# Optimization experiments

Hardware: AMD Instinct MI355X
Metric: run time of the kernel (lower is better)

## Reference

```python
import jax, jax.numpy as jnp
import numpy as np

HIDDEN = 1024
N_HEADS = 16
HEAD_DIM = HIDDEN // N_HEADS


def setup_inputs() -> dict:
    key = jax.random.key(0)
    ks = jax.random.split(key, 9)
    s = 1.0 / np.sqrt(HIDDEN)
    d = {"hidden_states": jax.random.normal(ks[0], (2, 2048, HIDDEN), dtype=jnp.float32)}
    for i, name in enumerate(["q", "k", "v", "o"]):
        d[f"W{name}"] = jax.random.uniform(ks[1 + 2 * i], (HIDDEN, HIDDEN), minval=-s, maxval=s, dtype=jnp.float32)
        d[f"b{name}"] = jax.random.uniform(ks[2 + 2 * i], (HIDDEN,), minval=-s, maxval=s, dtype=jnp.float32)
    return d


def reference(hidden_states, Wq, bq, Wk, bk, Wv, bv, Wo, bo):
    B, L, _ = hidden_states.shape

    def shape(x):  # (B, L, H*D) -> (B, H, L, D)
        return x.reshape(B, L, N_HEADS, HEAD_DIM).transpose(0, 2, 1, 3)

    q = shape(hidden_states @ Wq.T + bq)
    k = shape(hidden_states @ Wk.T + bk)
    v = shape(hidden_states @ Wv.T + bv)
    scores = jnp.einsum("bhqd,bhkd->bhqk", q, k) / jnp.sqrt(jnp.float32(HEAD_DIM))
    attn = jax.nn.softmax(scores, axis=-1)
    ctx = jnp.einsum("bhqk,bhkd->bhqd", attn, v)
    ctx = ctx.transpose(0, 2, 1, 3).reshape(B, L, HIDDEN)
    return ctx @ Wo.T + bo
```

## Files before the change

kernel.cpp:

```cpp
#include <hip/hip_runtime.h>
#include <hip/hip_bf16.h>
#include <stdint.h>

typedef __bf16 bf16_t;
typedef __bf16 bf16x8 __attribute__((ext_vector_type(8)));
typedef __bf16 bf16x4 __attribute__((ext_vector_type(4)));
typedef float  f32x4  __attribute__((ext_vector_type(4)));
typedef float  f32x16 __attribute__((ext_vector_type(16)));

__device__ __forceinline__ f32x4 mfma16(bf16x8 a, bf16x8 b, f32x4 c) {
    return __builtin_amdgcn_mfma_f32_16x16x32_bf16(a, b, c, 0, 0, 0);
}
__device__ __forceinline__ f32x16 mfma32(bf16x8 a, bf16x8 b, f32x16 c) {
    return __builtin_amdgcn_mfma_f32_32x32x16_bf16(a, b, c, 0, 0, 0);
}
__device__ __forceinline__ void gload16(const void* g, void* l) {
    __builtin_amdgcn_global_load_lds(
        (const __attribute__((address_space(1))) unsigned int*)g,
        (__attribute__((address_space(3))) unsigned int*)l, 16, 0, 0);
}
__device__ __forceinline__ unsigned cvtpk(float lo, float hi_) {
    unsigned r;
    asm("v_cvt_pk_bf16_f32 %0, %1, %2" : "=v"(r) : "v"(lo), "v"(hi_));
    return r;
}
__device__ __forceinline__ float fexp2(float x) {
    return __builtin_amdgcn_exp2f(x);
}

__global__ __launch_bounds__(256) void split_x(const float* __restrict__ in,
                                               bf16_t* __restrict__ hi, int n8) {
    int i = blockIdx.x * 256 + threadIdx.x;
    if (i >= n8) return;
    int row = i >> 7;
    int di = (i & ~3) | ((i & 3) ^ ((row >> 1) & 3));
    const float4* in4 = reinterpret_cast<const float4*>(in);
    float4 v0 = in4[2 * i], v1 = in4[2 * i + 1];
    float vv[8] = {v0.x, v0.y, v0.z, v0.w, v1.x, v1.y, v1.z, v1.w};
    bf16x8 h;
#pragma unroll
    for (int j = 0; j < 8; ++j) h[j] = (bf16_t)vv[j];
    reinterpret_cast<bf16x8*>(hi)[di] = h;
}

__global__ __launch_bounds__(256) void split_w(const float* __restrict__ w0, const float* __restrict__ w1,
                                               const float* __restrict__ w2, const float* __restrict__ w3,
                                               bf16_t* __restrict__ h0, bf16_t* __restrict__ h1,
                                               bf16_t* __restrict__ h2, bf16_t* __restrict__ h3) {
    int s = blockIdx.y;
    const float* in = (s == 0) ? w0 : (s == 1) ? w1 : (s == 2) ? w2 : w3;
    bf16_t* hi = (s == 0) ? h0 : (s == 1) ? h1 : (s == 2) ? h2 : h3;
    int i = blockIdx.x * 256 + threadIdx.x;
    int row = i >> 7;
    int di = (i & ~3) | ((i & 3) ^ ((row >> 1) & 3));
    const float4* in4 = reinterpret_cast<const float4*>(in);
    float4 v0 = in4[2 * i], v1 = in4[2 * i + 1];
    float vv[8] = {v0.x, v0.y, v0.z, v0.w, v1.x, v1.y, v1.z, v1.w};
    bf16x8 h;
#pragma unroll
    for (int j = 0; j < 8; ++j) h[j] = (bf16_t)vv[j];
    reinterpret_cast<bf16x8*>(hi)[di] = h;
}

__global__ __launch_bounds__(512) void gemm_qkv(const bf16_t* __restrict__ Xhi,
                                                const bf16_t* __restrict__ Wqh,
                                                const bf16_t* __restrict__ Wkh,
                                                const bf16_t* __restrict__ Wvh,
                                                const float* __restrict__ bq, const float* __restrict__ bk,
                                                const float* __restrict__ bv,
                                                bf16_t* __restrict__ Qb, bf16_t* __restrict__ Kb,
                                                bf16_t* __restrict__ Vt) {
    __shared__ alignas(16) bf16_t ldsA[2][128 * 32];
    __shared__ alignas(16) bf16_t ldsB[2][128 * 32];
    const int tid = threadIdx.x, wave = tid >> 6, lane = tid & 63;
    const int g = lane >> 4, cc = lane & 15;
    const int bx = blockIdx.x, which = bx >> 3;
    const bf16_t* Bh = (which == 0) ? Wqh : (which == 1) ? Wkh : Wvh;
    const float* bias = (which == 0) ? bq : (which == 1) ? bk : bv;
    const float scale = (which == 0) ? 0.125f * 1.4426950408889634f : 1.0f;
    const int mBase = blockIdx.y * 128, nB = (bx & 7) * 128;
    const int wm = wave >> 2, wn = wave & 3;

    f32x4 zero = {0.f, 0.f, 0.f, 0.f};
    f32x4 acc[4][2];
#pragma unroll
    for (int mi = 0; mi < 4; ++mi)
#pragma unroll
        for (int ni = 0; ni < 2; ++ni) acc[mi][ni] = zero;

    auto stage = [&](int k0, int buf) {
#pragma unroll
        for (int i = 0; i < 2; ++i) {
            int c = wave + 8 * i;
            int tile = c >> 3, sub = c & 7;
            int row = sub * 16 + (lane >> 2);
            int colE = (lane & 3) * 8;
            const bf16_t* src = (tile == 0) ? Xhi + (size_t)(mBase + row) * 1024 + k0 + colE
                                            : Bh + (size_t)(nB + row) * 1024 + k0 + colE;
            bf16_t* dst = (tile == 0) ? ldsA[buf] : ldsB[buf];
            gload16(src, (char*)dst + sub * 1024);
        }
    };

    stage(0, 0);
    for (int t = 0; t < 32; ++t) {
        const int buf = t & 1;
        if (t < 31) {
            stage((t + 1) * 32, buf ^ 1);
            asm volatile("s_waitcnt vmcnt(2)" ::: "memory");
        } else {
            asm volatile("s_waitcnt vmcnt(0)" ::: "memory");
        }
        __builtin_amdgcn_s_barrier();
        __builtin_amdgcn_sched_barrier(0);
        {
            bf16x8 af[4], bf_[2];
#pragma unroll
            for (int mi = 0; mi < 4; ++mi) {
                int ra = wm * 64 + mi * 16 + cc;
                af[mi] = *reinterpret_cast<const bf16x8*>(
                    (const char*)ldsA[buf] + ra * 64 + ((g ^ ((ra >> 1) & 3)) * 16));
            }
#pragma unroll
            for (int ni = 0; ni < 2; ++ni) {
                int rb = wn * 32 + ni * 16 + cc;
                bf_[ni] = *reinterpret_cast<const bf16x8*>(
                    (const char*)ldsB[buf] + rb * 64 + ((g ^ ((rb >> 1) & 3)) * 16));
            }
#pragma unroll
            for (int mi = 0; mi < 4; ++mi)
#pragma unroll
                for (int ni = 0; ni < 2; ++ni)
                    acc[mi][ni] = mfma16(af[mi], bf_[ni], acc[mi][ni]);
        }
        __builtin_amdgcn_s_barrier();
    }

#pragma unroll
    for (int mi = 0; mi < 4; ++mi)
#pragma unroll
        for (int ni = 0; ni < 2; ++ni)
#pragma unroll
            for (int r = 0; r < 4; ++r) {
                int row = mBase + wm * 64 + mi * 16 + g * 4 + r;
                int colL = nB + wn * 32 + ni * 16 + cc;
                float v = (acc[mi][ni][r] + bias[colL]) * scale;
                int b = row >> 11, tok = row & 2047, h = colL >> 6, d = colL & 63;
                if (which == 2) {
                    int kt = tok >> 6, key = tok & 63;
                    size_t o = (((size_t)(b * 16 + h) * 32 + kt) * 4096)
                             + d * 64 + ((((key >> 3) ^ (d & 7)) << 3) | (key & 7));
                    Vt[o] = (bf16_t)v;
                } else {
                    int dd = (which == 1) ? ((((d >> 3) ^ (tok & 7)) << 3) | (d & 7)) : d;
                    bf16_t* out = (which == 0) ? Qb : Kb;
                    out[((size_t)(b * 16 + h) * 2048 + tok) * 64 + dd] = (bf16_t)v;
                }
            }
}

__global__ __launch_bounds__(512) void gemm_o(const bf16_t* __restrict__ Ahi,
                                              const bf16_t* __restrict__ Bhi,
                                              const float* __restrict__ bias,
                                              float* __restrict__ outF) {
    __shared__ alignas(16) bf16_t ldsA[2][64 * 32];
    __shared__ alignas(16) bf16_t ldsB[2][128 * 32];
    const int tid = threadIdx.x, wave = tid >> 6, lane = tid & 63;
    const int g = lane >> 4, cc = lane & 15;
    const int mBase = blockIdx.y * 64, nBase = blockIdx.x * 128;
    const int wm = wave >> 2, wn = wave & 3;

    f32x4 zero = {0.f, 0.f, 0.f, 0.f};
    f32x4 acc[2][2];
#pragma unroll
    for (int mi = 0; mi < 2; ++mi)
#pragma unroll
        for (int ni = 0; ni < 2; ++ni) acc[mi][ni] = zero;

    auto stage = [&](int k0, int buf) {
#pragma unroll
        for (int i = 0; i < 2; ++i) {
            int c = wave + 8 * i;
            if (c >= 12) continue;
            const bf16_t* srcb;
            bf16_t* dst;
            int sub, rbase;
            if (c < 4) { srcb = Ahi; dst = ldsA[buf]; sub = c;     rbase = mBase; }
            else       { srcb = Bhi; dst = ldsB[buf]; sub = c - 4; rbase = nBase; }
            int row = sub * 16 + (lane >> 2);
            int colE = (lane & 3) * 8;
            gload16(srcb + (size_t)(rbase + row) * 1024 + k0 + colE, (char*)dst + sub * 1024);
        }
    };

    stage(0, 0);
    for (int t = 0; t < 32; ++t) {
        const int buf = t & 1;
        if (t < 31) {
            stage((t + 1) * 32, buf ^ 1);
            if (wave < 4) asm volatile("s_waitcnt vmcnt(2)" ::: "memory");
            else          asm volatile("s_waitcnt vmcnt(1)" ::: "memory");
        } else {
            asm volatile("s_waitcnt vmcnt(0)" ::: "memory");
        }
        __builtin_amdgcn_s_barrier();
        __builtin_amdgcn_sched_barrier(0);
        {
            bf16x8 af[2], bf_[2];
#pragma unroll
            for (int mi = 0; mi < 2; ++mi) {
                int ra = wm * 32 + mi * 16 + cc;
                af[mi] = *reinterpret_cast<const bf16x8*>(
                    (const char*)ldsA[buf] + ra * 64 + ((g ^ ((ra >> 1) & 3)) * 16));
            }
#pragma unroll
            for (int ni = 0; ni < 2; ++ni) {
                int rb = wn * 32 + ni * 16 + cc;
                bf_[ni] = *reinterpret_cast<const bf16x8*>(
                    (const char*)ldsB[buf] + rb * 64 + ((g ^ ((rb >> 1) & 3)) * 16));
            }
#pragma unroll
            for (int mi = 0; mi < 2; ++mi)
#pragma unroll
                for (int ni = 0; ni < 2; ++ni)
                    acc[mi][ni] = mfma16(af[mi], bf_[ni], acc[mi][ni]);
        }
        __builtin_amdgcn_s_barrier();
    }

#pragma unroll
    for (int mi = 0; mi < 2; ++mi)
#pragma unroll
        for (int ni = 0; ni < 2; ++ni)
#pragma unroll
            for (int r = 0; r < 4; ++r) {
                int row = mBase + wm * 32 + mi * 16 + g * 4 + r;
                int col = nBase + wn * 32 + ni * 16 + cc;
                outF[(size_t)row * 1024 + col] = acc[mi][ni][r] + bias[col];
            }
}

__global__ __launch_bounds__(512, 4) void attn_kernel(const bf16_t* __restrict__ Qb,
                                                      const bf16_t* __restrict__ Kb_p,
                                                      const bf16_t* __restrict__ Vt_p,
                                                      bf16_t* __restrict__ ctxHi) {
    __shared__ alignas(16) bf16_t SB[2][16384];

    const int lid = blockIdx.x;
    const int xcd = lid & 7, slot = lid >> 3;
    const int bh = xcd * 4 + (slot & 3);
    const int qt = slot >> 2;

    const int tid = threadIdx.x, w = tid >> 6, l = tid & 63;
    const int ql = l & 31, hi = l >> 5;
    const int wq = w & 3;
    const int par = w >> 2;
    const size_t kbase = (size_t)bh * 2048 * 64;
    const unsigned rsw = (unsigned)(ql & 7) << 4;

    bf16x8 qf[4];
    {
        const bf16_t* qp = Qb + kbase + (size_t)(qt * 128 + wq * 32 + ql) * 64 + hi * 8;
#pragma unroll
        for (int c = 0; c < 4; ++c) qf[c] = *reinterpret_cast<const bf16x8*>(qp + c * 16);
    }
    bf16x8 ones;
#pragma unroll
    for (int j = 0; j < 8; ++j) ones[j] = (bf16_t)1.0f;

    f32x16 O0{}, O1{}, Lacc{};

    auto stage = [&](int r) {
        int buf = r & 1;
        const bf16_t* ks = Kb_p + kbase + (size_t)(2 * r) * 4096;
        const bf16_t* vs = Vt_p + ((size_t)bh * 32 + 2 * r) * 4096;
        char* kd = (char*)&SB[buf][0];
        char* vd = (char*)&SB[buf][8192];
        gload16(ks + (size_t)tid * 8,        kd + tid * 16);
        gload16(ks + (size_t)tid * 8 + 4096, kd + tid * 16 + 8192);
        gload16(vs + (size_t)tid * 8,        vd + tid * 16);
        gload16(vs + (size_t)tid * 8 + 4096, vd + tid * 16 + 8192);
    };

    stage(0);

    for (int r = 0; r < 16; ++r) {
        const int buf = r & 1;
        if (r < 15) {
            stage(r + 1);
            asm volatile("s_waitcnt vmcnt(4)" ::: "memory");
        } else {
            asm volatile("s_waitcnt vmcnt(0)" ::: "memory");
        }
        __builtin_amdgcn_s_barrier();
        __builtin_amdgcn_sched_barrier(0);

        const char* kb = (const char*)&SB[buf][par * 4096];
        const char* vb = (const char*)&SB[buf][8192 + par * 4096];

        f32x16 S0{}, S1{};
        __builtin_amdgcn_s_setprio(1);
#pragma unroll
        for (int c = 0; c < 4; ++c) {
            unsigned col = ((unsigned)(c * 32 + hi * 16)) ^ rsw;
            bf16x8 k0 = *reinterpret_cast<const bf16x8*>(kb + (unsigned)ql * 128 + col);
            bf16x8 k1 = *reinterpret_cast<const bf16x8*>(kb + (unsigned)(32 + ql) * 128 + col);
            S0 = mfma32(k0, qf[c], S0);
            S1 = mfma32(k1, qf[c], S1);
        }
        __builtin_amdgcn_s_setprio(0);

#pragma unroll
        for (int r2 = 0; r2 < 16; ++r2) {
            S0[r2] = fexp2(S0[r2]);
            S1[r2] = fexp2(S1[r2]);
        }

        union U { unsigned u[4]; bf16x8 v; };
        bf16x8 PB[4];
#define MKFRAG(DST, SS, M8)                                                       \
        {                                                                         \
            unsigned c0 = cvtpk(SS[M8 + 0], SS[M8 + 1]);                          \
            unsigned c1 = cvtpk(SS[M8 + 2], SS[M8 + 3]);                          \
            unsigned c2 = cvtpk(SS[M8 + 4], SS[M8 + 5]);                          \
            unsigned c3 = cvtpk(SS[M8 + 6], SS[M8 + 7]);                          \
            unsigned y0 = hi ? c0 : c2;                                           \
            unsigned y1 = hi ? c1 : c3;                                           \
            unsigned z0 = (unsigned)__shfl_xor((int)y0, 32);                      \
            unsigned z1 = (unsigned)__shfl_xor((int)y1, 32);                      \
            U uu;                                                                 \
            uu.u[0] = hi ? z0 : c0;                                               \
            uu.u[1] = hi ? z1 : c1;                                               \
            uu.u[2] = hi ? c2 : z0;                                               \
            uu.u[3] = hi ? c3 : z1;                                               \
            DST = uu.v;                                                           \
        }
        MKFRAG(PB[0], S0, 0)
        MKFRAG(PB[1], S0, 8)
        MKFRAG(PB[2], S1, 0)
        MKFRAG(PB[3], S1, 8)
#undef MKFRAG

        __builtin_amdgcn_s_setprio(1);
#pragma unroll
        for (int ks = 0; ks < 4; ++ks) {
            unsigned col = ((unsigned)(ks * 32 + hi * 16)) ^ rsw;
            bf16x8 v0 = *reinterpret_cast<const bf16x8*>(vb + (unsigned)ql * 128 + col);
            bf16x8 v1 = *reinterpret_cast<const bf16x8*>(vb + (unsigned)(32 + ql) * 128 + col);
            O0 = mfma32(v0, PB[ks], O0);
            O1 = mfma32(v1, PB[ks], O1);
            Lacc = mfma32(ones, PB[ks], Lacc);
        }
        __builtin_amdgcn_s_setprio(0);

        __builtin_amdgcn_s_barrier();
    }

    float lsum = Lacc[0];
    float* mbuf = (float*)&SB[0][0];
    if (par == 1) {
        float* p = mbuf + (size_t)(wq * 64 + l) * 36;
        p[0] = lsum;
#pragma unroll
        for (int r2 = 0; r2 < 16; ++r2) { p[1 + r2] = O0[r2]; p[17 + r2] = O1[r2]; }
    }
    __syncthreads();
    if (par == 1) return;

    {
        const float* p = mbuf + (size_t)(wq * 64 + l) * 36;
        lsum += p[0];
#pragma unroll
        for (int r2 = 0; r2 < 16; ++r2) {
            O0[r2] += p[1 + r2];
            O1[r2] += p[17 + r2];
        }
    }

    const int b = bh >> 4, h = bh & 15;
    const int ltok = qt * 128 + wq * 32 + ql;
    const float inv = 1.0f / lsum;
    bf16_t* baseH = ctxHi + ((size_t)(b * 2048 + ltok)) * 1024 + h * 64;
    const int rsw4 = (ql >> 1) & 3;
#define WRITE4(OT, RQ, DT)                                                      \
    {                                                                           \
        int d0 = (RQ ^ rsw4) * 8 + 4 * hi + 32 * DT;                            \
        bf16x4 vh;                                                              \
        _Pragma("unroll")                                                       \
        for (int i = 0; i < 4; ++i) {                                           \
            float v = OT[4 * RQ + i] * inv;                                     \
            vh[i] = (bf16_t)v;                                                  \
        }                                                                       \
        *reinterpret_cast<bf16x4*>(baseH + d0) = vh;                            \
    }
    WRITE4(O0, 0, 0) WRITE4(O0, 1, 0) WRITE4(O0, 2, 0) WRITE4(O0, 3, 0)
    WRITE4(O1, 0, 1) WRITE4(O1, 1, 1) WRITE4(O1, 2, 1) WRITE4(O1, 3, 1)
#undef WRITE4
}

extern "C" void kernel_launch(void* const* d_in, const int* in_sizes, int n_in,
                              void* d_out, int out_size, void* d_ws, size_t ws_size,
                              hipStream_t stream) {
    const float* X  = (const float*)d_in[0];
    const float* Wq = (const float*)d_in[1];
    const float* bq = (const float*)d_in[2];
    const float* Wk = (const float*)d_in[3];
    const float* bk = (const float*)d_in[4];
    const float* Wv = (const float*)d_in[5];
    const float* bv = (const float*)d_in[6];
    const float* Wo = (const float*)d_in[7];
    const float* bo = (const float*)d_in[8];

    const size_t MB = 1024 * 1024;
    char* ws = (char*)d_ws;
    bf16_t* Xhi = (bf16_t*)(ws);
    bf16_t* Wqh = (bf16_t*)(ws + 8 * MB);
    bf16_t* Wkh = (bf16_t*)(ws + 10 * MB);
    bf16_t* Wvh = (bf16_t*)(ws + 12 * MB);
    bf16_t* Woh = (bf16_t*)(ws + 14 * MB);
    bf16_t* Qb  = (bf16_t*)(ws + 24 * MB);
    bf16_t* Kb  = (bf16_t*)(ws + 32 * MB);
    bf16_t* Vt  = (bf16_t*)(ws + 40 * MB);
    bf16_t* Chi = (bf16_t*)(ws + 48 * MB);

    split_x<<<2048, 256, 0, stream>>>(X, Xhi, 4194304 / 8);
    dim3 wGrid(512, 4);
    split_w<<<wGrid, 256, 0, stream>>>(Wq, Wk, Wv, Wo,
                                       Wqh, Wkh, Wvh, Woh);

    dim3 qkvGrid(24, 32);
    gemm_qkv<<<qkvGrid, 512, 0, stream>>>(Xhi, Wqh, Wkh, Wvh,
                                          bq, bk, bv, Qb, Kb, Vt);

    attn_kernel<<<512, 512, 0, stream>>>(Qb, Kb, Vt, Chi);

    dim3 oGrid(8, 64);
    gemm_o<<<oGrid, 512, 0, stream>>>(Chi, Woh, bo, (float*)d_out);
}
```

Baseline: 112.7 us.

## Merge split kernels and restructure double-buffer sync to one barrier per step

Combines the X and weight bf16 conversion kernels into a single launch to save one kernel launch. In both GEMMs and the attention kernel, the prefetch of the next tile now issues after a full vmcnt(0) wait and barrier, which lets the trailing per-iteration barrier be dropped. Prefetch no longer overlaps the wait for the current tile, so memory latency may be exposed more. The attention merge buffer stride also changes from 36 to 33 floats, likely to reduce LDS bank conflicts.

New measurement: 112.4 us. About the same (-0.3%).

```diff
diff --git a/kernel.cpp b/kernel.cpp
--- a/kernel.cpp
+++ b/kernel.cpp
@@ -28,29 +28,25 @@
     return __builtin_amdgcn_exp2f(x);
 }
 
-__global__ __launch_bounds__(256) void split_x(const float* __restrict__ in,
-                                               bf16_t* __restrict__ hi, int n8) {
-    int i = blockIdx.x * 256 + threadIdx.x;
-    if (i >= n8) return;
-    int row = i >> 7;
-    int di = (i & ~3) | ((i & 3) ^ ((row >> 1) & 3));
-    const float4* in4 = reinterpret_cast<const float4*>(in);
-    float4 v0 = in4[2 * i], v1 = in4[2 * i + 1];
-    float vv[8] = {v0.x, v0.y, v0.z, v0.w, v1.x, v1.y, v1.z, v1.w};
-    bf16x8 h;
-#pragma unroll
-    for (int j = 0; j < 8; ++j) h[j] = (bf16_t)vv[j];
-    reinterpret_cast<bf16x8*>(hi)[di] = h;
-}
-
-__global__ __launch_bounds__(256) void split_w(const float* __restrict__ w0, const float* __restrict__ w1,
-                                               const float* __restrict__ w2, const float* __restrict__ w3,
-                                               bf16_t* __restrict__ h0, bf16_t* __restrict__ h1,
-                                               bf16_t* __restrict__ h2, bf16_t* __restrict__ h3) {
-    int s = blockIdx.y;
-    const float* in = (s == 0) ? w0 : (s == 1) ? w1 : (s == 2) ? w2 : w3;
-    bf16_t* hi = (s == 0) ? h0 : (s == 1) ? h1 : (s == 2) ? h2 : h3;
-    int i = blockIdx.x * 256 + threadIdx.x;
+__global__ __launch_bounds__(256) void split_all(const float* __restrict__ X,
+                                                 const float* __restrict__ w0, const float* __restrict__ w1,
+                                                 const float* __restrict__ w2, const float* __restrict__ w3,
+                                                 bf16_t* __restrict__ xh,
+                                                 bf16_t* __restrict__ h0, bf16_t* __restrict__ h1,
+                                                 bf16_t* __restrict__ h2, bf16_t* __restrict__ h3) {
+    int blk = blockIdx.x;
+    const float* in;
+    bf16_t* hi;
+    int i;
+    if (blk < 2048) {
+        in = X; hi = xh;
+        i = blk * 256 + threadIdx.x;
+    } else {
+        int s = (blk - 2048) >> 9;
+        in = (s == 0) ? w0 : (s == 1) ? w1 : (s == 2) ? w2 : w3;
+        hi = (s == 0) ? h0 : (s == 1) ? h1 : (s == 2) ? h2 : h3;
+        i = ((blk - 2048) & 511) * 256 + threadIdx.x;
+    }
     int row = i >> 7;
     int di = (i & ~3) | ((i & 3) ^ ((row >> 1) & 3));
     const float4* in4 = reinterpret_cast<const float4*>(in);
@@ -105,14 +101,10 @@
     stage(0, 0);
     for (int t = 0; t < 32; ++t) {
         const int buf = t & 1;
-        if (t < 31) {
-            stage((t + 1) * 32, buf ^ 1);
-            asm volatile("s_waitcnt vmcnt(2)" ::: "memory");
-        } else {
-            asm volatile("s_waitcnt vmcnt(0)" ::: "memory");
-        }
+        asm volatile("s_waitcnt vmcnt(0)" ::: "memory");
         __builtin_amdgcn_s_barrier();
         __builtin_amdgcn_sched_barrier(0);
+        if (t < 31) stage((t + 1) * 32, buf ^ 1);
         {
             bf16x8 af[4], bf_[2];
 #pragma unroll
@@ -133,7 +125,6 @@
                 for (int ni = 0; ni < 2; ++ni)
                     acc[mi][ni] = mfma16(af[mi], bf_[ni], acc[mi][ni]);
         }
-        __builtin_amdgcn_s_barrier();
     }
 
 #pragma unroll
@@ -196,15 +187,10 @@
     stage(0, 0);
     for (int t = 0; t < 32; ++t) {
         const int buf = t & 1;
-        if (t < 31) {
-            stage((t + 1) * 32, buf ^ 1);
-            if (wave < 4) asm volatile("s_waitcnt vmcnt(2)" ::: "memory");
-            else          asm volatile("s_waitcnt vmcnt(1)" ::: "memory");
-        } else {
-            asm volatile("s_waitcnt vmcnt(0)" ::: "memory");
-        }
+        asm volatile("s_waitcnt vmcnt(0)" ::: "memory");
         __builtin_amdgcn_s_barrier();
         __builtin_amdgcn_sched_barrier(0);
+        if (t < 31) stage((t + 1) * 32, buf ^ 1);
         {
             bf16x8 af[2], bf_[2];
 #pragma unroll
@@ -225,7 +211,6 @@
                 for (int ni = 0; ni < 2; ++ni)
                     acc[mi][ni] = mfma16(af[mi], bf_[ni], acc[mi][ni]);
         }
-        __builtin_amdgcn_s_barrier();
     }
 
 #pragma unroll
@@ -286,14 +271,10 @@
 
     for (int r = 0; r < 16; ++r) {
         const int buf = r & 1;
-        if (r < 15) {
-            stage(r + 1);
-            asm volatile("s_waitcnt vmcnt(4)" ::: "memory");
-        } else {
-            asm volatile("s_waitcnt vmcnt(0)" ::: "memory");
-        }
+        asm volatile("s_waitcnt vmcnt(0)" ::: "memory");
         __builtin_amdgcn_s_barrier();
         __builtin_amdgcn_sched_barrier(0);
+        if (r < 15) stage(r + 1);
 
         const char* kb = (const char*)&SB[buf][par * 4096];
         const char* vb = (const char*)&SB[buf][8192 + par * 4096];
@@ -352,14 +333,14 @@
             Lacc = mfma32(ones, PB[ks], Lacc);
         }
         __builtin_amdgcn_s_setprio(0);
-
-        __builtin_amdgcn_s_barrier();
-    }
+    }
+
+    __builtin_amdgcn_s_barrier();
 
     float lsum = Lacc[0];
     float* mbuf = (float*)&SB[0][0];
     if (par == 1) {
-        float* p = mbuf + (size_t)(wq * 64 + l) * 36;
+        float* p = mbuf + (size_t)(wq * 64 + l) * 33;
         p[0] = lsum;
 #pragma unroll
         for (int r2 = 0; r2 < 16; ++r2) { p[1 + r2] = O0[r2]; p[17 + r2] = O1[r2]; }
@@ -368,7 +349,7 @@
     if (par == 1) return;
 
     {
-        const float* p = mbuf + (size_t)(wq * 64 + l) * 36;
+        const float* p = mbuf + (size_t)(wq * 64 + l) * 33;
         lsum += p[0];
 #pragma unroll
         for (int r2 = 0; r2 < 16; ++r2) {
@@ -423,10 +404,8 @@
     bf16_t* Vt  = (bf16_t*)(ws + 40 * MB);
     bf16_t* Chi = (bf16_t*)(ws + 48 * MB);
 
-    split_x<<<2048, 256, 0, stream>>>(X, Xhi, 4194304 / 8);
-    dim3 wGrid(512, 4);
-    split_w<<<wGrid, 256, 0, stream>>>(Wq, Wk, Wv, Wo,
-                                       Wqh, Wkh, Wvh, Woh);
+    split_all<<<4096, 256, 0, stream>>>(X, Wq, Wk, Wv, Wo,
+                                        Xhi, Wqh, Wkh, Wvh, Woh);
 
     dim3 qkvGrid(24, 32);
     gemm_qkv<<<qkvGrid, 512, 0, stream>>>(Xhi, Wqh, Wkh, Wvh,
```
